# Kernel optimization log

Measured on AMD Instinct MI355X. Metric: run time of the kernel, lower is better.

## Reference

```python
import jax, jax.numpy as jnp
import numpy as np
import math

N, C, W, H = 8, 1024, 1024, 16
D = C // H  # head size = 64


def setup_inputs() -> dict:
    key = jax.random.key(0)
    ks = jax.random.split(key, 7)
    s = 1.0 / math.sqrt(C)
    return {
        "hidden_states": jax.random.normal(ks[0], (N, C, W), jnp.float32),
        "attention_mask": jnp.zeros((N, 1, 1, W), jnp.float32),
        "wq": jax.random.normal(ks[1], (C, C), jnp.float32) * s,
        "bq": jax.random.normal(ks[2], (C,), jnp.float32) * 0.02,
        "wk": jax.random.normal(ks[3], (C, C), jnp.float32) * s,
        "bk": jax.random.normal(ks[4], (C,), jnp.float32) * 0.02,
        "wv": jax.random.normal(ks[5], (C, C), jnp.float32) * s,
        "bv": jax.random.normal(ks[6], (C,), jnp.float32) * 0.02,
    }


def reference(hidden_states, attention_mask, wq, bq, wk, bk, wv, bv):
    # conv1d(kernel=1, groups=1) == per-position GEMM: [N,C,W] x [Cout,Cin] -> [N,Cout,W]
    q = jnp.einsum('ncw,oc->now', hidden_states, wq) + bq[None, :, None]
    k = jnp.einsum('ncw,oc->now', hidden_states, wk) + bk[None, :, None]
    v = jnp.einsum('ncw,oc->now', hidden_states, wv) + bv[None, :, None]
    # split heads: [N,C,W] -> [N,H,D,W]
    q = q.reshape(N, H, D, W).transpose(0, 1, 3, 2)  # [N,H,W,D]
    k = k.reshape(N, H, D, W)                         # [N,H,D,W]
    v = v.reshape(N, H, D, W).transpose(0, 1, 3, 2)  # [N,H,W,D]
    scores = jnp.einsum('nhqd,nhdk->nhqk', q, k) / math.sqrt(D)
    scores = scores + attention_mask  # broadcast [N,1,1,W]
    probs = jax.nn.softmax(scores, axis=-1)
    ctx = jnp.einsum('nhqk,nhkd->nhqd', probs, v)    # [N,H,W,D]
    # merge heads back to [N,C,W]
    return ctx.transpose(0, 1, 3, 2).reshape(N, C, W)
```

## Files before the change

kernel.cpp:

```cpp
#include <hip/hip_runtime.h>
#include <hip/hip_bf16.h>

typedef __bf16 bf16x8 __attribute__((ext_vector_type(8)));
typedef __bf16 bf16x4 __attribute__((ext_vector_type(4)));
typedef float f32x4 __attribute__((ext_vector_type(4)));

#define N_ 8
#define C_ 1024
#define W_ 1024
#define H_ 16
#define D_ 64

typedef __attribute__((address_space(3))) void lds_void;
typedef const __attribute__((address_space(1))) void gbl_void;
static __device__ __forceinline__ void gload_lds16(const void* g, void* l) {
    __builtin_amdgcn_global_load_lds((gbl_void*)g, (lds_void*)l, 16, 0, 0);
}

__global__ __launch_bounds__(256)
void prep(const float* __restrict__ hs,
          const float* __restrict__ wq, const float* __restrict__ wk,
          const float* __restrict__ wv,
          __bf16* __restrict__ Xt, __bf16* __restrict__ Wb) {
    __shared__ float tile[64][68];
    const int b = blockIdx.x;
    const int t = threadIdx.x;
    if (b < 2048) {
        const int bx = b & 15, by = (b >> 4) & 15, bz = b >> 8;
        const long bin  = (long)bz * C_ * W_;
        const long bout = (long)bz * W_ * C_;
        const int w0 = bx * 64, c0 = by * 64;
        const int rr = t >> 4;
        const int cg = (t & 15) * 4;
        #pragma unroll
        for (int it = 0; it < 4; ++it) {
            const int cr = it * 16 + rr;
            f32x4 v = *(const f32x4*)(const void*)(hs + bin + (long)(c0 + cr) * W_ + w0 + cg);
            *(f32x4*)&tile[cr][cg] = v;
        }
        __syncthreads();
        #pragma unroll
        for (int it = 0; it < 4; ++it) {
            const int wr = it * 16 + rr;
            bf16x4 o;
            #pragma unroll
            for (int u = 0; u < 4; ++u) o[u] = (__bf16)tile[cg + u][wr];
            *(bf16x4*)(void*)(Xt + bout + (long)(w0 + wr) * C_ + c0 + cg) = o;
        }
    } else {
        const int cb = b - 2048;
        const int wsel = cb >> 9;
        const int x = cb & 511;
        const float* s = wsel == 0 ? wq : (wsel == 1 ? wk : wv);
        __bf16* d = Wb + (long)wsel * C_ * C_;
        const long i = ((long)x * 256 + t) * 8;
        f32x4 a = *(const f32x4*)(const void*)(s + i);
        f32x4 bb = *(const f32x4*)(const void*)(s + i + 4);
        bf16x8 v;
        #pragma unroll
        for (int u = 0; u < 4; ++u) { v[u] = (__bf16)a[u]; v[u + 4] = (__bf16)bb[u]; }
        *(bf16x8*)(void*)(d + i) = v;
    }
}

template<int OUT_T>
static __device__ __forceinline__
void gemm_body(const __bf16* __restrict__ Aw, const __bf16* __restrict__ Xn,
               const float* __restrict__ bias, __bf16* __restrict__ Pn,
               const int o0, const int w0,
               __bf16* __restrict__ As, __bf16* __restrict__ Bs) {
    const int tid = threadIdx.x;
    const int wv = tid >> 6, lane = tid & 63;
    const int l15 = lane & 15, quad = lane >> 4;
    const int wr = (wv >> 1) * 64, wc = (wv & 1) * 64;
    const int lr4 = lane >> 2;
    const int lc4 = lane & 3;

    f32x4 acc[4][4] = {};

    auto stage = [&](int k0, int b) {
        #pragma unroll
        for (int j = 0; j < 2; ++j) {
            const int seg = wv * 2 + j;
            const int r = seg * 16 + lr4;
            const int q = lc4 ^ ((lr4 >> 1) & 3);
            gload_lds16(Aw + (long)(o0 + r) * C_ + k0 + q * 8, As + b * 4096 + seg * 512);
            gload_lds16(Xn + (long)(w0 + r) * C_ + k0 + q * 8, Bs + b * 4096 + seg * 512);
        }
    };

    stage(0, 0);
    stage(32, 1);

    int cur = 0, nxt = 2;
    #pragma unroll 1
    for (int ti = 0; ti < 32; ++ti) {
        if (ti < 31) asm volatile("s_waitcnt vmcnt(4)" ::: "memory");
        else         asm volatile("s_waitcnt vmcnt(0)" ::: "memory");
        __builtin_amdgcn_s_barrier();
        asm volatile("" ::: "memory");
        if (ti + 2 < 32) {
            stage((ti + 2) * 32, nxt);
            nxt = nxt + 1 == 3 ? 0 : nxt + 1;
        }

        const __bf16* Ab = As + cur * 4096;
        const __bf16* Bb = Bs + cur * 4096;
        bf16x8 af[4], bf[4];
        #pragma unroll
        for (int mt = 0; mt < 4; ++mt) {
            const int R = wr + mt * 16 + l15;
            const int pos = quad ^ ((R >> 1) & 3);
            af[mt] = *(const bf16x8*)(const void*)&Ab[R * 32 + pos * 8];
        }
        #pragma unroll
        for (int nt = 0; nt < 4; ++nt) {
            const int R = wc + nt * 16 + l15;
            const int pos = quad ^ ((R >> 1) & 3);
            bf[nt] = *(const bf16x8*)(const void*)&Bb[R * 32 + pos * 8];
        }
        #pragma unroll
        for (int mt = 0; mt < 4; ++mt)
            #pragma unroll
            for (int nt = 0; nt < 4; ++nt) {
                if (OUT_T == 0)
                    acc[mt][nt] = __builtin_amdgcn_mfma_f32_16x16x32_bf16(af[mt], bf[nt], acc[mt][nt], 0, 0, 0);
                else
                    acc[mt][nt] = __builtin_amdgcn_mfma_f32_16x16x32_bf16(bf[nt], af[mt], acc[mt][nt], 0, 0, 0);
            }
        cur = cur + 1 == 3 ? 0 : cur + 1;
    }

    #pragma unroll
    for (int mt = 0; mt < 4; ++mt) {
        #pragma unroll
        for (int nt = 0; nt < 4; ++nt) {
            #pragma unroll
            for (int rg = 0; rg < 4; ++rg) {
                if (OUT_T == 0) {
                    const int col = w0 + wc + nt * 16 + l15;
                    const int row = o0 + wr + mt * 16 + quad * 4 + rg;
                    Pn[(long)row * W_ + col] = (__bf16)(acc[mt][nt][rg] + bias[row]);
                } else {
                    const int o = o0 + wr + mt * 16 + l15;
                    const int w = w0 + wc + nt * 16 + quad * 4 + rg;
                    Pn[(long)w * C_ + o] = (__bf16)(acc[mt][nt][rg] + bias[o]);
                }
            }
        }
    }
}

__global__ __launch_bounds__(256)
void gemm_qkv(const __bf16* __restrict__ Wb, const __bf16* __restrict__ Xt,
              const float* __restrict__ bq, const float* __restrict__ bk,
              const float* __restrict__ bv,
              __bf16* __restrict__ Qt, __bf16* __restrict__ Kt,
              __bf16* __restrict__ Vb) {
    __shared__ __align__(16) __bf16 As[3 * 4096];
    __shared__ __align__(16) __bf16 Bs[3 * 4096];
    const int f = blockIdx.x;
    const int n = f & 7;
    const int j = f >> 3;
    const int which = j >> 6;
    const int t = j & 63;
    const int o0 = (t >> 3) * 128;
    const int w0 = (t & 7) * 128;
    const size_t SZ = (size_t)C_ * W_;
    const size_t WSZ = (size_t)C_ * C_;
    const __bf16* Xn = Xt + (size_t)n * SZ;
    const __bf16* Aw = Wb + (size_t)which * WSZ;
    if (which < 2)
        gemm_body<1>(Aw, Xn, which ? bk : bq, (which ? Kt : Qt) + n * SZ, o0, w0, As, Bs);
    else
        gemm_body<0>(Aw, Xn, bv, Vb + n * SZ, o0, w0, As, Bs);
}

__global__ __launch_bounds__(256)
void flash_attn(const __bf16* __restrict__ Qt,
                const __bf16* __restrict__ Kt,
                const __bf16* __restrict__ V,
                const float* __restrict__ mask,
                float* __restrict__ out) {
    __shared__ __align__(16) __bf16 Pl[4 * 16 * 64];
    __shared__ __align__(16) __bf16 Ks[2][64 * 64];
    __shared__ __align__(16) __bf16 Vs[2][64 * 64];

    const int f = blockIdx.x;
    const int g = (f & 7) + ((f >> 6) << 3);
    const int m = (f >> 3) & 7;
    const int n = g >> 4, h = g & 15;
    const int q0 = m * 128;

    const int tid = threadIdx.x;
    const int wave = tid >> 6, lane = tid & 63;
    const int l15 = lane & 15, quad = lane >> 4;
    const int lr8 = lane >> 3, lp = lane & 7;
    const long nqk = (long)n * W_ * C_;
    const long nv = (long)n * C_ * W_;
    const int hD = h * D_;
    const float* mrow = mask + (long)n * W_;
    constexpr float SC = 0.125f * 1.44269504f;
    constexpr float L2E = 1.44269504f;

    char* plb = (char*)Pl + wave * 2048;
    const int swz = (l15 & 7) << 4;
    const int plrow = l15 * 128;

    bf16x8 aq[2][2];
    #pragma unroll
    for (int qs = 0; qs < 2; ++qs)
        #pragma unroll
        for (int dc = 0; dc < 2; ++dc)
            aq[qs][dc] = *(const bf16x8*)(const void*)
                (Qt + nqk + (long)(q0 + wave * 32 + qs * 16 + l15) * C_ + hD + dc * 32 + quad * 8);

    f32x4 o_acc[2][4] = {};
    float l_ln[2] = {};

    auto stage = [&](int kt, int b) {
        #pragma unroll
        for (int jj = 0; jj < 2; ++jj) {
            const int seg = wave * 2 + jj;
            const int r = seg * 8 + lr8;
            const int q = lp ^ (r & 7);
            gload_lds16(Kt + nqk + (long)(kt + r) * C_ + hD + q * 8, &Ks[b][seg * 512]);
            gload_lds16(V + nv + (long)(hD + r) * W_ + kt + q * 8, &Vs[b][seg * 512]);
        }
    };

    stage(0, 0);

    for (int ti = 0; ti < W_ / 64; ++ti) {
        const int kt = ti * 64;
        const int cur = ti & 1;
        asm volatile("s_waitcnt vmcnt(0)" ::: "memory");
        __syncthreads();
        if (ti + 1 < W_ / 64) stage(kt + 64, cur ^ 1);

        bf16x8 bk[4][2];
        #pragma unroll
        for (int ks = 0; ks < 4; ++ks)
            #pragma unroll
            for (int dc = 0; dc < 2; ++dc) {
                const int R = ks * 16 + l15;
                const int pos = (dc * 4 + quad) ^ (R & 7);
                bk[ks][dc] = *(const bf16x8*)(const void*)&Ks[cur][R * 64 + pos * 8];
            }
        f32x4 mk2[4];
        #pragma unroll
        for (int ks = 0; ks < 4; ++ks) {
            f32x4 mv = *(const f32x4*)(const void*)(mrow + kt + ks * 16 + quad * 4);
            #pragma unroll
            for (int rg = 0; rg < 4; ++rg) mk2[ks][rg] = mv[rg] * L2E;
        }

        f32x4 s2[2][4] = {};
        #pragma unroll
        for (int qs = 0; qs < 2; ++qs)
            #pragma unroll
            for (int ks = 0; ks < 4; ++ks)
                #pragma unroll
                for (int dc = 0; dc < 2; ++dc)
                    s2[qs][ks] = __builtin_amdgcn_mfma_f32_16x16x32_bf16(bk[ks][dc], aq[qs][dc], s2[qs][ks], 0, 0, 0);

        #pragma unroll
        for (int qs = 0; qs < 2; ++qs)
            #pragma unroll
            for (int ks = 0; ks < 4; ++ks) {
                #pragma unroll
                for (int rg = 0; rg < 4; ++rg)
                    s2[qs][ks][rg] = __builtin_amdgcn_exp2f(s2[qs][ks][rg] * SC + mk2[ks][rg]);
                l_ln[qs] += (s2[qs][ks][0] + s2[qs][ks][1]) + (s2[qs][ks][2] + s2[qs][ks][3]);
            }

        bf16x8 ap[2][2];
        #pragma unroll
        for (int qs = 0; qs < 2; ++qs) {
            #pragma unroll
            for (int ks = 0; ks < 4; ++ks) {
                bf16x4 p4;
                #pragma unroll
                for (int rg = 0; rg < 4; ++rg) p4[rg] = (__bf16)s2[qs][ks][rg];
                *(bf16x4*)(void*)(plb + plrow + ((ks * 32 + quad * 8) ^ swz)) = p4;
            }
            #pragma unroll
            for (int kc = 0; kc < 2; ++kc)
                ap[qs][kc] = *(const bf16x8*)(const void*)
                    (plb + plrow + ((kc * 64 + quad * 16) ^ swz));
        }

        bf16x8 bv[4][2];
        #pragma unroll
        for (int ds = 0; ds < 4; ++ds)
            #pragma unroll
            for (int kc = 0; kc < 2; ++kc) {
                const int R = ds * 16 + l15;
                const int pos = (kc * 4 + quad) ^ (R & 7);
                bv[ds][kc] = *(const bf16x8*)(const void*)&Vs[cur][R * 64 + pos * 8];
            }
        #pragma unroll
        for (int qs = 0; qs < 2; ++qs)
            #pragma unroll
            for (int ds = 0; ds < 4; ++ds)
                #pragma unroll
                for (int kc = 0; kc < 2; ++kc)
                    o_acc[qs][ds] = __builtin_amdgcn_mfma_f32_16x16x32_bf16(ap[qs][kc], bv[ds][kc], o_acc[qs][ds], 0, 0, 0);
    }

    #pragma unroll
    for (int qs = 0; qs < 2; ++qs) {
        float l = l_ln[qs];
        l += __shfl_xor(l, 16, 64);
        l += __shfl_xor(l, 32, 64);
        const float linv = 1.0f / l;
        #pragma unroll
        for (int rg = 0; rg < 4; ++rg) {
            const float inv = __shfl(linv, quad * 4 + rg, 64);
            #pragma unroll
            for (int ds = 0; ds < 4; ++ds)
                out[nv + (long)(hD + ds * 16 + l15) * W_ + q0 + wave * 32 + qs * 16 + quad * 4 + rg]
                    = o_acc[qs][ds][rg] * inv;
        }
    }
}

extern "C" void kernel_launch(void* const* d_in, const int* in_sizes, int n_in,
                              void* d_out, int out_size, void* d_ws, size_t ws_size,
                              hipStream_t stream) {
    (void)in_sizes; (void)n_in; (void)out_size; (void)ws_size;
    const float* hs   = (const float*)d_in[0];
    const float* mask = (const float*)d_in[1];
    const float* wq   = (const float*)d_in[2];
    const float* bq   = (const float*)d_in[3];
    const float* wk   = (const float*)d_in[4];
    const float* bk   = (const float*)d_in[5];
    const float* wv   = (const float*)d_in[6];
    const float* bv   = (const float*)d_in[7];
    float* out = (float*)d_out;

    const size_t SZ = (size_t)N_ * C_ * W_;
    const size_t WSZ = (size_t)C_ * C_;
    __bf16* Wb = (__bf16*)d_ws;
    __bf16* Xt = Wb + 3 * WSZ;
    __bf16* Qt = Xt + SZ;
    __bf16* Kt = Qt + SZ;
    __bf16* Vb = Kt + SZ;

    prep<<<dim3(2048 + 1536), 256, 0, stream>>>(hs, wq, wk, wv, Xt, Wb);

    gemm_qkv<<<dim3(1536), 256, 0, stream>>>(Wb, Xt, bq, bk, bv, Qt, Kt, Vb);

    flash_attn<<<dim3(1024), 256, 0, stream>>>(Qt, Kt, Vb, mask, out);
}
```

Baseline: 232.6 us.

## Load GEMM weights straight to registers and split K/V staging in attention

```diff
diff --git a/kernel.cpp b/kernel.cpp
--- a/kernel.cpp
+++ b/kernel.cpp
@@ -67,8 +67,7 @@
 static __device__ __forceinline__
 void gemm_body(const __bf16* __restrict__ Aw, const __bf16* __restrict__ Xn,
                const float* __restrict__ bias, __bf16* __restrict__ Pn,
-               const int o0, const int w0,
-               __bf16* __restrict__ As, __bf16* __restrict__ Bs) {
+               const int o0, const int w0, __bf16* __restrict__ Bs) {
     const int tid = threadIdx.x;
     const int wv = tid >> 6, lane = tid & 63;
     const int l15 = lane & 15, quad = lane >> 4;
@@ -78,41 +77,41 @@
 
     f32x4 acc[4][4] = {};
 
-    auto stage = [&](int k0, int b) {
+    auto stageB = [&](int k0, int b) {
         #pragma unroll
         for (int j = 0; j < 2; ++j) {
             const int seg = wv * 2 + j;
             const int r = seg * 16 + lr4;
             const int q = lc4 ^ ((lr4 >> 1) & 3);
-            gload_lds16(Aw + (long)(o0 + r) * C_ + k0 + q * 8, As + b * 4096 + seg * 512);
             gload_lds16(Xn + (long)(w0 + r) * C_ + k0 + q * 8, Bs + b * 4096 + seg * 512);
         }
     };
 
-    stage(0, 0);
-    stage(32, 1);
+    stageB(0, 0);
+    stageB(32, 1);
 
     int cur = 0, nxt = 2;
     #pragma unroll 1
     for (int ti = 0; ti < 32; ++ti) {
-        if (ti < 31) asm volatile("s_waitcnt vmcnt(4)" ::: "memory");
+        if (ti < 31) asm volatile("s_waitcnt vmcnt(2)" ::: "memory");
         else         asm volatile("s_waitcnt vmcnt(0)" ::: "memory");
         __builtin_amdgcn_s_barrier();
         asm volatile("" ::: "memory");
+
+        const int k0 = ti * 32;
+        bf16x8 af[4];
+        #pragma unroll
+        for (int mt = 0; mt < 4; ++mt) {
+            const int R = o0 + wr + mt * 16 + l15;
+            af[mt] = *(const bf16x8*)(const void*)(Aw + (long)R * C_ + k0 + quad * 8);
+        }
         if (ti + 2 < 32) {
-            stage((ti + 2) * 32, nxt);
+            stageB((ti + 2) * 32, nxt);
             nxt = nxt + 1 == 3 ? 0 : nxt + 1;
         }
 
-        const __bf16* Ab = As + cur * 4096;
         const __bf16* Bb = Bs + cur * 4096;
-        bf16x8 af[4], bf[4];
-        #pragma unroll
-        for (int mt = 0; mt < 4; ++mt) {
-            const int R = wr + mt * 16 + l15;
-            const int pos = quad ^ ((R >> 1) & 3);
-            af[mt] = *(const bf16x8*)(const void*)&Ab[R * 32 + pos * 8];
-        }
+        bf16x8 bf[4];
         #pragma unroll
         for (int nt = 0; nt < 4; ++nt) {
             const int R = wc + nt * 16 + l15;
@@ -157,7 +156,6 @@
               const float* __restrict__ bv,
               __bf16* __restrict__ Qt, __bf16* __restrict__ Kt,
               __bf16* __restrict__ Vb) {
-    __shared__ __align__(16) __bf16 As[3 * 4096];
     __shared__ __align__(16) __bf16 Bs[3 * 4096];
     const int f = blockIdx.x;
     const int n = f & 7;
@@ -171,9 +169,9 @@
     const __bf16* Xn = Xt + (size_t)n * SZ;
     const __bf16* Aw = Wb + (size_t)which * WSZ;
     if (which < 2)
-        gemm_body<1>(Aw, Xn, which ? bk : bq, (which ? Kt : Qt) + n * SZ, o0, w0, As, Bs);
+        gemm_body<1>(Aw, Xn, which ? bk : bq, (which ? Kt : Qt) + n * SZ, o0, w0, Bs);
     else
-        gemm_body<0>(Aw, Xn, bv, Vb + n * SZ, o0, w0, As, Bs);
+        gemm_body<0>(Aw, Xn, bv, Vb + n * SZ, o0, w0, Bs);
 }
 
 __global__ __launch_bounds__(256)
@@ -218,25 +216,37 @@
     f32x4 o_acc[2][4] = {};
     float l_ln[2] = {};
 
-    auto stage = [&](int kt, int b) {
+    auto stageK = [&](int kt, int b) {
         #pragma unroll
         for (int jj = 0; jj < 2; ++jj) {
             const int seg = wave * 2 + jj;
             const int r = seg * 8 + lr8;
             const int q = lp ^ (r & 7);
             gload_lds16(Kt + nqk + (long)(kt + r) * C_ + hD + q * 8, &Ks[b][seg * 512]);
+        }
+    };
+    auto stageV = [&](int kt, int b) {
+        #pragma unroll
+        for (int jj = 0; jj < 2; ++jj) {
+            const int seg = wave * 2 + jj;
+            const int r = seg * 8 + lr8;
+            const int q = lp ^ (r & 7);
             gload_lds16(V + nv + (long)(hD + r) * W_ + kt + q * 8, &Vs[b][seg * 512]);
         }
     };
 
-    stage(0, 0);
-
+    stageK(0, 0);
+    stageV(0, 0);
+
+    #pragma unroll 1
     for (int ti = 0; ti < W_ / 64; ++ti) {
         const int kt = ti * 64;
         const int cur = ti & 1;
-        asm volatile("s_waitcnt vmcnt(0)" ::: "memory");
-        __syncthreads();
-        if (ti + 1 < W_ / 64) stage(kt + 64, cur ^ 1);
+
+        asm volatile("s_waitcnt vmcnt(2)" ::: "memory");
+        __builtin_amdgcn_s_barrier();
+        asm volatile("" ::: "memory");
+        if (ti + 1 < W_ / 64) stageK(kt + 64, cur ^ 1);
 
         bf16x8 bk[4][2];
         #pragma unroll
@@ -289,6 +299,12 @@
                 ap[qs][kc] = *(const bf16x8*)(const void*)
                     (plb + plrow + ((kc * 64 + quad * 16) ^ swz));
         }
+
+        if (ti + 1 < W_ / 64) asm volatile("s_waitcnt vmcnt(2)" ::: "memory");
+        else                  asm volatile("s_waitcnt vmcnt(0)" ::: "memory");
+        __builtin_amdgcn_s_barrier();
+        asm volatile("" ::: "memory");
+        if (ti + 1 < W_ / 64) stageV(kt + 64, cur ^ 1);
 
         bf16x8 bv[4][2];
         #pragma unroll
```

Measured after the change: 272.7 us. +17.2%, slower.
